# Optimization experiments

Hardware: AMD Instinct MI355X
Metric: run time of the kernel (lower is better)

Reference implementation:

```python
import jax, jax.numpy as jnp
import numpy as np

N_NODES = 200_000
N_EDGES = 6_400_000
F_IN = 16


def mish(x):
    return x * jnp.tanh(jax.nn.softplus(x))


def setup_inputs() -> dict:
    key = jax.random.key(0)
    ks = jax.random.split(key, 10)

    def glorot(k, shape):
        lim = np.sqrt(6.0 / (shape[0] + shape[1]))
        return jax.random.uniform(k, shape, jnp.float32, -lim, lim)

    return {
        "x": jax.random.normal(ks[0], (N_NODES, F_IN), jnp.float32),
        "edge_index": jax.random.randint(ks[1], (2, N_EDGES), 0, N_NODES, dtype=jnp.int32),
        "W1": glorot(ks[2], (F_IN, 8)),
        "b1": jnp.zeros((8,), jnp.float32),
        "W2": glorot(ks[3], (8, 16)),
        "b2": jnp.zeros((16,), jnp.float32),
        "W3": glorot(ks[4], (16, 8)),
        "b3": jnp.zeros((8,), jnp.float32),
        "W4": glorot(ks[5], (8, 2)),
        "b4": jnp.zeros((2,), jnp.float32),
    }


def reference(x, edge_index, W1, b1, W2, b2, W3, b3, W4, b4):
    # GCN with 4 GCNConv layers, Mish between layers, LogSoftmax output.
    # Dropout is identity in eval mode and omitted.
    N = x.shape[0]
    loops = jnp.arange(N, dtype=edge_index.dtype)
    src = jnp.concatenate([edge_index[0], loops])  # add self-loops once
    dst = jnp.concatenate([edge_index[1], loops])

    # symmetric normalization: deg computed over destination (PyG convention)
    deg = jax.ops.segment_sum(jnp.ones_like(dst, dtype=x.dtype), dst, num_segments=N)
    dinv = jax.lax.rsqrt(jnp.maximum(deg, 1.0))  # deg >= 1 because of self-loops
    norm = dinv[src] * dinv[dst]                 # [E + N]

    def conv(h, W, b):
        hW = h @ W                               # [N, F_out]
        msg = hW[src] * norm[:, None]            # gather + scale
        return jax.ops.segment_sum(msg, dst, num_segments=N) + b

    h = mish(conv(x, W1, b1))
    h = mish(conv(h, W2, b2))
    h = mish(conv(h, W3, b3))
    h = conv(h, W4, b4)
    return jax.nn.log_softmax(h, axis=1)
```

## Files before the change

### kernel.cpp

```cpp
#include <hip/hip_runtime.h>
#include <hip/hip_fp16.h>
#include <math.h>

static constexpr int NN = 200000;
static constexpr int NE = 6400000;
static constexpr int TB = 256;
static constexpr int NBUCK = (NN + 255) / 256;
static constexpr int CAP = 10240;
static constexpr int CH = 8192;
static constexpr int NCHUNK = (NE + CH - 1) / CH;


__device__ __forceinline__ float2 h2f(int b) {
    union { int i; __half2 h; } u; u.i = b;
    return __half22float2(u.h);
}
__device__ __forceinline__ int f2h(float a, float b) {
    union { __half2 h; int i; } u; u.h = __floats2half2_rn(a, b);
    return u.i;
}
__device__ __forceinline__ void acc8(const int4 r, float* acc) {
    float2 f;
    f = h2f(r.x); acc[0] += f.x; acc[1] += f.y;
    f = h2f(r.y); acc[2] += f.x; acc[3] += f.y;
    f = h2f(r.z); acc[4] += f.x; acc[5] += f.y;
    f = h2f(r.w); acc[6] += f.x; acc[7] += f.y;
}
__device__ __forceinline__ int4 pack8(const float* o) {
    int4 r;
    r.x = f2h(o[0], o[1]); r.y = f2h(o[2], o[3]);
    r.z = f2h(o[4], o[5]); r.w = f2h(o[6], o[7]);
    return r;
}

__device__ __forceinline__ float mishf(float x) {
    float sp = (x > 20.f) ? x : log1pf(expf(x));
    return x * tanhf(sp);
}


__global__ __launch_bounds__(TB) void k_bin(const int* __restrict__ src, const int* __restrict__ dst,
                                            int* __restrict__ gcur, int* __restrict__ csr) {
    __shared__ int hist[NBUCK];
    __shared__ int scn[NBUCK];
    __shared__ int gb[NBUCK];
    __shared__ int stage[CH];
    __shared__ unsigned short bkt[CH];
    int t = threadIdx.x;
    int e0 = blockIdx.x * CH;
    int n = min(CH, NE - e0);

    for (int j = t; j < NBUCK; j += TB) hist[j] = 0;
    __syncthreads();
    for (int j = t; j < n; j += TB)
        atomicAdd(&hist[dst[e0 + j] >> 8], 1);
    __syncthreads();
    for (int j = t; j < NBUCK; j += TB) scn[j] = hist[j];
    __syncthreads();
    for (int off = 1; off < NBUCK; off <<= 1) {
        int v[4];
#pragma unroll
        for (int k = 0; k < 4; ++k) {
            int idx = t + k * TB;
            v[k] = (idx < NBUCK && idx >= off) ? scn[idx - off] : 0;
        }
        __syncthreads();
#pragma unroll
        for (int k = 0; k < 4; ++k) {
            int idx = t + k * TB;
            if (idx < NBUCK) scn[idx] += v[k];
        }
        __syncthreads();
    }
    for (int j = t; j < NBUCK; j += TB) {
        int c = hist[j];
        int excl = scn[j] - c;
        int gbase = c ? atomicAdd(&gcur[j], c) : 0;
        gb[j] = j * CAP + gbase - excl;
        scn[j] = excl;
    }
    __syncthreads();
    for (int j = t; j < n; j += TB) {
        int d = dst[e0 + j];
        int s = src[e0 + j];
        int b = d >> 8;
        int pos = atomicAdd(&scn[b], 1);
        stage[pos] = (s << 8) | (d & 255);
        bkt[pos] = (unsigned short)b;
    }
    __syncthreads();
    for (int j = t; j < n; j += TB) {
        int b = bkt[j];
        int dest = gb[b] + j;
        if (dest < (b + 1) * CAP)
            csr[dest] = stage[j];
    }
}

__global__ __launch_bounds__(TB) void k_group(const int* __restrict__ gcur, int* __restrict__ csr,
                                              unsigned* __restrict__ meta, float* __restrict__ dinv,
                                              int* __restrict__ dh,
                                              const float* __restrict__ x, const float* __restrict__ W1,
                                              int4* __restrict__ T1) {
    __shared__ int hist[TB];
    __shared__ int scn[TB];
    __shared__ int cur[TB];
    __shared__ int grp[CAP];
    int t = threadIdx.x;
    int b = blockIdx.x;
    int base = b * CAP;
    int nE = min(gcur[b], CAP);
    hist[t] = 0; cur[t] = 0;
    __syncthreads();
    for (int j = t; j < nE; j += TB)
        atomicAdd(&hist[csr[base + j] & 255], 1);
    __syncthreads();
    int deg = hist[t];
    scn[t] = deg;
    __syncthreads();
#pragma unroll
    for (int o = 1; o < TB; o <<= 1) {
        int u = (t >= o) ? scn[t - o] : 0;
        __syncthreads();
        scn[t] += u;
        __syncthreads();
    }
    int off = scn[t] - deg;
    int node = b * 256 + t;
    int degc = min(deg, 255);
    float di = rsqrtf((float)(deg + 1));
    if (node < NN) {
        meta[node] = ((unsigned)(base + off) << 8) | (unsigned)degc;
        dinv[node] = di;
    }
    hist[t] = off;
    __syncthreads();
    for (int j = t; j < nE; j += TB) {
        int p = csr[base + j];
        int dl = p & 255;
        int l = atomicAdd(&cur[dl], 1);
        grp[hist[dl] + l] = p >> 8;
    }
    __syncthreads();
    for (int j = t; j < nE; j += TB) csr[base + j] = grp[j];

    __syncthreads();
    cur[t] = 0;
    __syncthreads();
    if (node < NN) atomicAdd(&cur[degc], 1);
    __syncthreads();
    if (cur[t]) atomicAdd(&dh[t], cur[t]);

    if (node >= NN) return;
    float in[16];
    const float4* hp = (const float4*)(x + (size_t)node * 16);
#pragma unroll
    for (int q = 0; q < 4; ++q) {
        float4 v = hp[q];
        in[4*q+0] = v.x; in[4*q+1] = v.y; in[4*q+2] = v.z; in[4*q+3] = v.w;
    }
    float o[8];
#pragma unroll
    for (int f = 0; f < 8; ++f) o[f] = 0.f;
#pragma unroll
    for (int k = 0; k < 16; ++k)
#pragma unroll
        for (int f = 0; f < 8; ++f) o[f] = fmaf(in[k], W1[k * 8 + f], o[f]);
#pragma unroll
    for (int f = 0; f < 8; ++f) o[f] *= di;
    T1[node] = pack8(o);
}


__global__ void k_dscan(const int* __restrict__ dh, int* __restrict__ dcur) {
    __shared__ int sm[256];
    int t = threadIdx.x;
    int v = dh[t];
    sm[t] = v;
    __syncthreads();
    for (int o = 1; o < 256; o <<= 1) {
        int u = (t >= o) ? sm[t - o] : 0;
        __syncthreads();
        sm[t] += u;
        __syncthreads();
    }
    int total = sm[255];
    dcur[t] = total - sm[t];
}

__global__ __launch_bounds__(TB) void k_dperm(const unsigned* __restrict__ meta, int* __restrict__ dcur,
                                              int* __restrict__ perm) {
    __shared__ int lh[256];
    __shared__ int lbase[256];
    __shared__ int lcur[256];
    int t = threadIdx.x;
    int node = blockIdx.x * TB + t;
    lh[t] = 0; lcur[t] = 0;
    __syncthreads();
    int deg = 0;
    if (node < NN) {
        deg = (int)(meta[node] & 255u);
        atomicAdd(&lh[deg], 1);
    }
    __syncthreads();
    int c = lh[t];
    lbase[t] = c ? atomicAdd(&dcur[t], c) : 0;
    __syncthreads();
    if (node < NN) {
        int slot = lbase[deg] + atomicAdd(&lcur[deg], 1);
        perm[slot] = node;
    }
}


template<int MODE>
__global__ __launch_bounds__(TB) void k_gather8(const int4* __restrict__ tab, const int* __restrict__ perm,
                                                const unsigned* __restrict__ meta,
                                                const int* __restrict__ csr, const float* __restrict__ dinv,
                                                const float* __restrict__ P0, const float* __restrict__ P1,
                                                const float* __restrict__ P2,
                                                int4* __restrict__ outH, int* __restrict__ out2) {
    int tid = blockIdx.x * TB + threadIdx.x;
    int pid = tid >> 2;
    int lane = tid & 3;
    if (pid >= NN) return;
    int node = perm[pid];
    unsigned m = meta[node];
    int start = (int)(m >> 8);
    int deg = (int)(m & 255u);
    const int* cp = csr + start;
    float acc[8];
#pragma unroll
    for (int f = 0; f < 8; ++f) acc[f] = 0.f;
    if (lane == 0) acc8(tab[node], acc);
    int e = lane;
    for (; e + 12 < deg; e += 16) {
        int s0 = cp[e];
        int s1 = cp[e + 4];
        int s2 = cp[e + 8];
        int s3 = cp[e + 12];
        int4 r0 = tab[s0];
        int4 r1 = tab[s1];
        int4 r2 = tab[s2];
        int4 r3 = tab[s3];
        acc8(r0, acc); acc8(r1, acc); acc8(r2, acc); acc8(r3, acc);
    }
    for (; e + 4 < deg; e += 8) {
        int s0 = cp[e];
        int s1 = cp[e + 4];
        int4 r0 = tab[s0];
        int4 r1 = tab[s1];
        acc8(r0, acc); acc8(r1, acc);
    }
    for (; e < deg; e += 4) {
        acc8(tab[cp[e]], acc);
    }
#pragma unroll
    for (int f = 0; f < 8; ++f) {
        acc[f] += __shfl_xor(acc[f], 1);
        acc[f] += __shfl_xor(acc[f], 2);
    }
    if (lane != 0) return;
    float di = dinv[node];
    if constexpr (MODE == 1) {
        float o[8];
#pragma unroll
        for (int f = 0; f < 8; ++f) o[f] = mishf(fmaf(acc[f], di, P0[f])) * di;
        outH[node] = pack8(o);
    } else if constexpr (MODE == 2) {
        float z[8];
#pragma unroll
        for (int f = 0; f < 8; ++f) z[f] = acc[f] * di;
        float h[16];
#pragma unroll
        for (int g = 0; g < 16; ++g) h[g] = P1[g];
#pragma unroll
        for (int f = 0; f < 8; ++f)
#pragma unroll
            for (int g = 0; g < 16; ++g) h[g] = fmaf(z[f], P0[f * 16 + g], h[g]);
#pragma unroll
        for (int g = 0; g < 16; ++g) h[g] = mishf(h[g]);
        float o[8];
#pragma unroll
        for (int q = 0; q < 8; ++q) o[q] = 0.f;
#pragma unroll
        for (int g = 0; g < 16; ++g)
#pragma unroll
            for (int q = 0; q < 8; ++q) o[q] = fmaf(h[g], P2[g * 8 + q], o[q]);
#pragma unroll
        for (int q = 0; q < 8; ++q) o[q] *= di;
        outH[node] = pack8(o);
    } else {
        float t8[8];
#pragma unroll
        for (int f = 0; f < 8; ++f) t8[f] = mishf(fmaf(acc[f], di, P0[f]));
        float o0 = 0.f, o1 = 0.f;
#pragma unroll
        for (int f = 0; f < 8; ++f) {
            o0 = fmaf(t8[f], P1[f * 2 + 0], o0);
            o1 = fmaf(t8[f], P1[f * 2 + 1], o1);
        }
        out2[node] = f2h(o0 * di, o1 * di);
    }
}

__global__ __launch_bounds__(TB) void k_gather2(const int* __restrict__ g, const int* __restrict__ perm,
                                                const unsigned* __restrict__ meta,
                                                const int* __restrict__ csr, const float* __restrict__ dinv,
                                                const float* __restrict__ b4, float* __restrict__ outp) {
    int tid = blockIdx.x * TB + threadIdx.x;
    int pid = tid >> 2;
    int lane = tid & 3;
    if (pid >= NN) return;
    int node = perm[pid];
    unsigned m = meta[node];
    int start = (int)(m >> 8);
    int deg = (int)(m & 255u);
    const int* cp = csr + start;
    float a0 = 0.f, a1 = 0.f;
    if (lane == 0) {
        float2 v = h2f(g[node]);
        a0 = v.x; a1 = v.y;
    }
    int e = lane;
    for (; e + 12 < deg; e += 16) {
        int s0 = cp[e];
        int s1 = cp[e + 4];
        int s2 = cp[e + 8];
        int s3 = cp[e + 12];
        float2 v0 = h2f(g[s0]); float2 v1 = h2f(g[s1]);
        float2 v2 = h2f(g[s2]); float2 v3 = h2f(g[s3]);
        a0 += v0.x + v1.x + v2.x + v3.x;
        a1 += v0.y + v1.y + v2.y + v3.y;
    }
    for (; e + 4 < deg; e += 8) {
        int s0 = cp[e];
        int s1 = cp[e + 4];
        float2 v0 = h2f(g[s0]);
        float2 v1 = h2f(g[s1]);
        a0 += v0.x + v1.x; a1 += v0.y + v1.y;
    }
    for (; e < deg; e += 4) {
        float2 v = h2f(g[cp[e]]);
        a0 += v.x; a1 += v.y;
    }
    a0 += __shfl_xor(a0, 1); a0 += __shfl_xor(a0, 2);
    a1 += __shfl_xor(a1, 1); a1 += __shfl_xor(a1, 2);
    if (lane != 0) return;
    float di = dinv[node];
    float z0 = fmaf(a0, di, b4[0]);
    float z1 = fmaf(a1, di, b4[1]);
    float mx = fmaxf(z0, z1);
    float l = mx + logf(expf(z0 - mx) + expf(z1 - mx));
    outp[(size_t)node * 2 + 0] = z0 - l;
    outp[(size_t)node * 2 + 1] = z1 - l;
}


extern "C" void kernel_launch(void* const* d_in, const int* in_sizes, int n_in,
                              void* d_out, int out_size, void* d_ws, size_t ws_size,
                              hipStream_t stream) {
    const float* x   = (const float*)d_in[0];
    const int*   ei  = (const int*)d_in[1];
    const int*   src = ei;
    const int*   dst = ei + NE;
    const float* W1 = (const float*)d_in[2];
    const float* b1 = (const float*)d_in[3];
    const float* W2 = (const float*)d_in[4];
    const float* b2 = (const float*)d_in[5];
    const float* W3 = (const float*)d_in[6];
    const float* b3 = (const float*)d_in[7];
    const float* W4 = (const float*)d_in[8];
    const float* b4 = (const float*)d_in[9];
    float* out = (float*)d_out;

    char* ws = (char*)d_ws;
    size_t off_b = 0;
    auto alloc = [&](size_t bytes) -> void* {
        off_b = (off_b + 255) & ~(size_t)255;
        void* p = ws + off_b;
        off_b += bytes;
        return p;
    };
    int*      gcur = (int*)     alloc((size_t)NBUCK * 4);
    int*      dh   = (int*)     alloc(256 * 4);
    int*      dcur = (int*)     alloc(256 * 4);
    unsigned* meta = (unsigned*)alloc((size_t)NN * 4);
    float*    dinv = (float*)   alloc((size_t)NN * 4);
    int*      perm = (int*)     alloc((size_t)NN * 4);
    int*      csr  = (int*)     alloc((size_t)NBUCK * CAP * 4);
    int4*     HA   = (int4*)    alloc((size_t)NN * 16);
    int4*     HB   = (int4*)    alloc((size_t)NN * 16);
    int*      T4   = (int*)     alloc((size_t)NN * 4);
    (void)ws_size;

    const int gG = (NN * 4 + TB - 1) / TB;
    const int gP = (NN + TB - 1) / TB;

    hipMemsetAsync(gcur, 0, (size_t)NBUCK * 4, stream);
    hipMemsetAsync(dh, 0, 256 * 4, stream);
    k_bin<<<NCHUNK, TB, 0, stream>>>(src, dst, gcur, csr);
    k_group<<<NBUCK, TB, 0, stream>>>(gcur, csr, meta, dinv, dh, x, W1, HA);

    k_dscan<<<1, 256, 0, stream>>>(dh, dcur);
    k_dperm<<<gP, TB, 0, stream>>>(meta, dcur, perm);

    k_gather8<1><<<gG, TB, 0, stream>>>(HA, perm, meta, csr, dinv, b1, nullptr, nullptr, HB, nullptr);
    k_gather8<2><<<gG, TB, 0, stream>>>(HB, perm, meta, csr, dinv, W2, b2, W3, HA, nullptr);
    k_gather8<3><<<gG, TB, 0, stream>>>(HA, perm, meta, csr, dinv, b3, W4, nullptr, nullptr, T4);
    k_gather2<<<gG, TB, 0, stream>>>(T4, perm, meta, csr, dinv, b4, out);
}
```

Before: 382.4 us.

## Split 8-wide feature gathers into two 4-wide passes for cache locality

Each 8-feature aggregation layer is split into two kernels that gather 4 half-precision features each from separate half-size tables. The first writes float4 partial sums, and the second combines them and applies the layer epilogue. The intent is to halve the random-gather working set so it stays in cache. In exchange, the CSR index stream is read twice per layer, a partial buffer is written and read, and extra kernel launches are added.

```diff
diff --git a/kernel.cpp b/kernel.cpp
--- a/kernel.cpp
+++ b/kernel.cpp
@@ -19,18 +19,13 @@
     union { __half2 h; int i; } u; u.h = __floats2half2_rn(a, b);
     return u.i;
 }
-__device__ __forceinline__ void acc8(const int4 r, float* acc) {
+__device__ __forceinline__ void acc4(const int2 r, float* a) {
     float2 f;
-    f = h2f(r.x); acc[0] += f.x; acc[1] += f.y;
-    f = h2f(r.y); acc[2] += f.x; acc[3] += f.y;
-    f = h2f(r.z); acc[4] += f.x; acc[5] += f.y;
-    f = h2f(r.w); acc[6] += f.x; acc[7] += f.y;
-}
-__device__ __forceinline__ int4 pack8(const float* o) {
-    int4 r;
-    r.x = f2h(o[0], o[1]); r.y = f2h(o[2], o[3]);
-    r.z = f2h(o[4], o[5]); r.w = f2h(o[6], o[7]);
-    return r;
+    f = h2f(r.x); a[0] += f.x; a[1] += f.y;
+    f = h2f(r.y); a[2] += f.x; a[3] += f.y;
+}
+__device__ __forceinline__ int2 pack4(float o0, float o1, float o2, float o3) {
+    return make_int2(f2h(o0, o1), f2h(o2, o3));
 }
 
 __device__ __forceinline__ float mishf(float x) {
@@ -101,7 +96,7 @@
                                               unsigned* __restrict__ meta, float* __restrict__ dinv,
                                               int* __restrict__ dh,
                                               const float* __restrict__ x, const float* __restrict__ W1,
-                                              int4* __restrict__ T1) {
+                                              int2* __restrict__ pA, int2* __restrict__ pB) {
     __shared__ int hist[TB];
     __shared__ int scn[TB];
     __shared__ int cur[TB];
@@ -168,7 +163,8 @@
         for (int f = 0; f < 8; ++f) o[f] = fmaf(in[k], W1[k * 8 + f], o[f]);
 #pragma unroll
     for (int f = 0; f < 8; ++f) o[f] *= di;
-    T1[node] = pack8(o);
+    pA[node] = pack4(o[0], o[1], o[2], o[3]);
+    pB[node] = pack4(o[4], o[5], o[6], o[7]);
 }
 
 
@@ -213,13 +209,10 @@
 }
 
 
-template<int MODE>
-__global__ __launch_bounds__(TB) void k_gather8(const int4* __restrict__ tab, const int* __restrict__ perm,
-                                                const unsigned* __restrict__ meta,
-                                                const int* __restrict__ csr, const float* __restrict__ dinv,
-                                                const float* __restrict__ P0, const float* __restrict__ P1,
-                                                const float* __restrict__ P2,
-                                                int4* __restrict__ outH, int* __restrict__ out2) {
+__global__ __launch_bounds__(TB) void k_gA(const int2* __restrict__ tab, const int* __restrict__ perm,
+                                           const unsigned* __restrict__ meta,
+                                           const int* __restrict__ csr,
+                                           float4* __restrict__ part) {
     int tid = blockIdx.x * TB + threadIdx.x;
     int pid = tid >> 2;
     int lane = tid & 3;
@@ -229,44 +222,93 @@
     int start = (int)(m >> 8);
     int deg = (int)(m & 255u);
     const int* cp = csr + start;
-    float acc[8];
-#pragma unroll
-    for (int f = 0; f < 8; ++f) acc[f] = 0.f;
-    if (lane == 0) acc8(tab[node], acc);
+    float a[4] = {0.f, 0.f, 0.f, 0.f};
+    if (lane == 0) acc4(tab[node], a);
     int e = lane;
     for (; e + 12 < deg; e += 16) {
         int s0 = cp[e];
         int s1 = cp[e + 4];
         int s2 = cp[e + 8];
         int s3 = cp[e + 12];
-        int4 r0 = tab[s0];
-        int4 r1 = tab[s1];
-        int4 r2 = tab[s2];
-        int4 r3 = tab[s3];
-        acc8(r0, acc); acc8(r1, acc); acc8(r2, acc); acc8(r3, acc);
+        int2 r0 = tab[s0];
+        int2 r1 = tab[s1];
+        int2 r2 = tab[s2];
+        int2 r3 = tab[s3];
+        acc4(r0, a); acc4(r1, a); acc4(r2, a); acc4(r3, a);
     }
     for (; e + 4 < deg; e += 8) {
         int s0 = cp[e];
         int s1 = cp[e + 4];
-        int4 r0 = tab[s0];
-        int4 r1 = tab[s1];
-        acc8(r0, acc); acc8(r1, acc);
-    }
-    for (; e < deg; e += 4) {
-        acc8(tab[cp[e]], acc);
-    }
-#pragma unroll
-    for (int f = 0; f < 8; ++f) {
-        acc[f] += __shfl_xor(acc[f], 1);
-        acc[f] += __shfl_xor(acc[f], 2);
+        int2 r0 = tab[s0];
+        int2 r1 = tab[s1];
+        acc4(r0, a); acc4(r1, a);
+    }
+    for (; e < deg; e += 4)
+        acc4(tab[cp[e]], a);
+#pragma unroll
+    for (int f = 0; f < 4; ++f) {
+        a[f] += __shfl_xor(a[f], 1);
+        a[f] += __shfl_xor(a[f], 2);
+    }
+    if (lane == 0) part[node] = make_float4(a[0], a[1], a[2], a[3]);
+}
+
+template<int MODE>
+__global__ __launch_bounds__(TB) void k_gB(const int2* __restrict__ tab, const int* __restrict__ perm,
+                                           const unsigned* __restrict__ meta,
+                                           const int* __restrict__ csr, const float* __restrict__ dinv,
+                                           const float4* __restrict__ part,
+                                           const float* __restrict__ P0, const float* __restrict__ P1,
+                                           const float* __restrict__ P2,
+                                           int2* __restrict__ outA, int2* __restrict__ outB,
+                                           int* __restrict__ out2) {
+    int tid = blockIdx.x * TB + threadIdx.x;
+    int pid = tid >> 2;
+    int lane = tid & 3;
+    if (pid >= NN) return;
+    int node = perm[pid];
+    unsigned m = meta[node];
+    int start = (int)(m >> 8);
+    int deg = (int)(m & 255u);
+    const int* cp = csr + start;
+    float a[4] = {0.f, 0.f, 0.f, 0.f};
+    if (lane == 0) acc4(tab[node], a);
+    int e = lane;
+    for (; e + 12 < deg; e += 16) {
+        int s0 = cp[e];
+        int s1 = cp[e + 4];
+        int s2 = cp[e + 8];
+        int s3 = cp[e + 12];
+        int2 r0 = tab[s0];
+        int2 r1 = tab[s1];
+        int2 r2 = tab[s2];
+        int2 r3 = tab[s3];
+        acc4(r0, a); acc4(r1, a); acc4(r2, a); acc4(r3, a);
+    }
+    for (; e + 4 < deg; e += 8) {
+        int s0 = cp[e];
+        int s1 = cp[e + 4];
+        int2 r0 = tab[s0];
+        int2 r1 = tab[s1];
+        acc4(r0, a); acc4(r1, a);
+    }
+    for (; e < deg; e += 4)
+        acc4(tab[cp[e]], a);
+#pragma unroll
+    for (int f = 0; f < 4; ++f) {
+        a[f] += __shfl_xor(a[f], 1);
+        a[f] += __shfl_xor(a[f], 2);
     }
     if (lane != 0) return;
+    float4 p = part[node];
+    float acc[8] = { p.x, p.y, p.z, p.w, a[0], a[1], a[2], a[3] };
     float di = dinv[node];
     if constexpr (MODE == 1) {
         float o[8];
 #pragma unroll
         for (int f = 0; f < 8; ++f) o[f] = mishf(fmaf(acc[f], di, P0[f])) * di;
-        outH[node] = pack8(o);
+        outA[node] = pack4(o[0], o[1], o[2], o[3]);
+        outB[node] = pack4(o[4], o[5], o[6], o[7]);
     } else if constexpr (MODE == 2) {
         float z[8];
 #pragma unroll
@@ -289,7 +331,8 @@
             for (int q = 0; q < 8; ++q) o[q] = fmaf(h[g], P2[g * 8 + q], o[q]);
 #pragma unroll
         for (int q = 0; q < 8; ++q) o[q] *= di;
-        outH[node] = pack8(o);
+        outA[node] = pack4(o[0], o[1], o[2], o[3]);
+        outB[node] = pack4(o[4], o[5], o[6], o[7]);
     } else {
         float t8[8];
 #pragma unroll
@@ -389,8 +432,11 @@
     float*    dinv = (float*)   alloc((size_t)NN * 4);
     int*      perm = (int*)     alloc((size_t)NN * 4);
     int*      csr  = (int*)     alloc((size_t)NBUCK * CAP * 4);
-    int4*     HA   = (int4*)    alloc((size_t)NN * 16);
-    int4*     HB   = (int4*)    alloc((size_t)NN * 16);
+    int2*     A0   = (int2*)    alloc((size_t)NN * 8);
+    int2*     B0   = (int2*)    alloc((size_t)NN * 8);
+    int2*     A1   = (int2*)    alloc((size_t)NN * 8);
+    int2*     B1   = (int2*)    alloc((size_t)NN * 8);
+    float4*   part = (float4*)  alloc((size_t)NN * 16);
     int*      T4   = (int*)     alloc((size_t)NN * 4);
     (void)ws_size;
 
@@ -400,13 +446,19 @@
     hipMemsetAsync(gcur, 0, (size_t)NBUCK * 4, stream);
     hipMemsetAsync(dh, 0, 256 * 4, stream);
     k_bin<<<NCHUNK, TB, 0, stream>>>(src, dst, gcur, csr);
-    k_group<<<NBUCK, TB, 0, stream>>>(gcur, csr, meta, dinv, dh, x, W1, HA);
+    k_group<<<NBUCK, TB, 0, stream>>>(gcur, csr, meta, dinv, dh, x, W1, A0, B0);
 
     k_dscan<<<1, 256, 0, stream>>>(dh, dcur);
     k_dperm<<<gP, TB, 0, stream>>>(meta, dcur, perm);
 
-    k_gather8<1><<<gG, TB, 0, stream>>>(HA, perm, meta, csr, dinv, b1, nullptr, nullptr, HB, nullptr);
-    k_gather8<2><<<gG, TB, 0, stream>>>(HB, perm, meta, csr, dinv, W2, b2, W3, HA, nullptr);
-    k_gather8<3><<<gG, TB, 0, stream>>>(HA, perm, meta, csr, dinv, b3, W4, nullptr, nullptr, T4);
+    k_gA<<<gG, TB, 0, stream>>>(A0, perm, meta, csr, part);
+    k_gB<1><<<gG, TB, 0, stream>>>(B0, perm, meta, csr, dinv, part, b1, nullptr, nullptr, A1, B1, nullptr);
+
+    k_gA<<<gG, TB, 0, stream>>>(A1, perm, meta, csr, part);
+    k_gB<2><<<gG, TB, 0, stream>>>(B1, perm, meta, csr, dinv, part, W2, b2, W3, A0, B0, nullptr);
+
+    k_gA<<<gG, TB, 0, stream>>>(A0, perm, meta, csr, part);
+    k_gB<3><<<gG, TB, 0, stream>>>(B0, perm, meta, csr, dinv, part, b3, W4, nullptr, nullptr, nullptr, T4);
+
     k_gather2<<<gG, TB, 0, stream>>>(T4, perm, meta, csr, dinv, b4, out);
 }
```

Measured after the change: 475.4 us. 24.3% more time.
